# Performance work log

Hardware: AMD Instinct MI355X
Metric: run time of the kernel (lower is better)

The kernel has to match this reference:

```python
import jax, jax.numpy as jnp
import numpy as np

B, S, D_IN, D_OUT = 4, 2048, 1024, 1024

def setup_inputs() -> dict:
    key = jax.random.key(0)
    ks = jax.random.split(key, 6)
    s = 1.0 / np.sqrt(D_IN)
    return {
        "inputs": jax.random.normal(ks[0], (B, S, D_IN), dtype=jnp.float32),
        "Wq": jax.random.normal(ks[1], (D_IN, D_OUT), dtype=jnp.float32) * s,
        "Wk": jax.random.normal(ks[2], (D_IN, D_OUT), dtype=jnp.float32) * s,
        "Wv": jax.random.normal(ks[3], (D_IN, D_OUT), dtype=jnp.float32) * s,
        "Wo": jax.random.normal(ks[4], (D_OUT, D_OUT), dtype=jnp.float32) * (1.0 / np.sqrt(D_OUT)),
        "bo": jax.random.normal(ks[5], (D_OUT,), dtype=jnp.float32) * 0.01,
    }

def reference(inputs, Wq, Wk, Wv, Wo, bo):
    # QKV projections (no bias, matching qkv_bias=False)
    q = inputs @ Wq  # [B,S,D]
    k = inputs @ Wk
    v = inputs @ Wv
    # naive full attention: scores [B,S,S]
    scores = jnp.einsum('bqd,bkd->bqk', q, k) / jnp.sqrt(jnp.asarray(k.shape[-1], q.dtype))
    attn = jax.nn.softmax(scores, axis=-1)
    out = jnp.einsum('bqk,bkd->bqd', attn, v)
    return out @ Wo + bo
```

## Files before the change

kernel.cpp:

```cpp
#include <hip/hip_runtime.h>
#include <hip/hip_bf16.h>
#include <cstdint>

typedef __attribute__((ext_vector_type(8))) __bf16 bf16x8;
typedef __attribute__((ext_vector_type(4))) float  f32x4;

__device__ __forceinline__ unsigned short f2bf(float x) {
    union { float f; unsigned u; } v; v.f = x;
    unsigned r = v.u + 0x7fffu + ((v.u >> 16) & 1u);
    return (unsigned short)(r >> 16);
}
__device__ __forceinline__ unsigned pack2bf(float a, float b) {
    return (unsigned)f2bf(a) | ((unsigned)f2bf(b) << 16);
}

__device__ __forceinline__ void gld_lds16(const unsigned short* g, unsigned short* l) {
    __builtin_amdgcn_global_load_lds(
        (const __attribute__((address_space(1))) unsigned int*)g,
        (__attribute__((address_space(3))) unsigned int*)l,
        16, 0, 0);
}

__global__ void cvt_kernel(const float* __restrict__ in, unsigned short* __restrict__ out, int n4) {
    int i = blockIdx.x * blockDim.x + threadIdx.x;
    if (i < n4) {
        float4 f = ((const float4*)in)[i];
        ushort4 o;
        o.x = f2bf(f.x); o.y = f2bf(f.y); o.z = f2bf(f.z); o.w = f2bf(f.w);
        ((ushort4*)out)[i] = o;
    }
}

__global__ void wpack_kernel(const float* __restrict__ W, unsigned short* __restrict__ out) {
    int tid  = threadIdx.x;
    int lane = tid & 63;
    int chunk = blockIdx.x * 4 + (tid >> 6);
    int nt = chunk >> 5, k32 = chunk & 31;
    int r = lane & 15, q = lane >> 4;
    const float* src = W + (size_t)(k32*32 + q*8) * 1024 + nt*16 + r;
    unsigned o[4];
#pragma unroll
    for (int i = 0; i < 4; i++)
        o[i] = pack2bf(src[(size_t)(2*i) * 1024], src[(size_t)(2*i+1) * 1024]);
    *(uint4*)(out + (size_t)chunk * 512 + lane * 8) = make_uint4(o[0], o[1], o[2], o[3]);
}

__global__ void softmax_kernel(unsigned short* __restrict__ S) {
    const size_t row = blockIdx.x;
    unsigned short* p = S + row * 2048;
    const int tid = threadIdx.x;
    const int wave = tid >> 6, lane = tid & 63;

    uint4 raw = ((const uint4*)p)[tid];
    unsigned u[4] = {raw.x, raw.y, raw.z, raw.w};
    float x[8];
#pragma unroll
    for (int i = 0; i < 4; i++) {
        x[2*i]   = __uint_as_float(u[i] << 16);
        x[2*i+1] = __uint_as_float(u[i] & 0xffff0000u);
    }
    float m = x[0];
#pragma unroll
    for (int i = 1; i < 8; i++) m = fmaxf(m, x[i]);
#pragma unroll
    for (int off = 32; off >= 1; off >>= 1) m = fmaxf(m, __shfl_xor(m, off, 64));
    __shared__ float sm[4], ss[4];
    if (lane == 0) sm[wave] = m;
    __syncthreads();
    m = fmaxf(fmaxf(sm[0], sm[1]), fmaxf(sm[2], sm[3]));

    float e[8], s = 0.f;
#pragma unroll
    for (int i = 0; i < 8; i++) { e[i] = __expf(x[i] - m); s += e[i]; }
#pragma unroll
    for (int off = 32; off >= 1; off >>= 1) s += __shfl_xor(s, off, 64);
    if (lane == 0) ss[wave] = s;
    __syncthreads();
    s = ss[0] + ss[1] + ss[2] + ss[3];
    float inv = 1.0f / s;

    unsigned o[4];
#pragma unroll
    for (int i = 0; i < 4; i++)
        o[i] = pack2bf(e[2*i] * inv, e[2*i+1] * inv);
    ((uint4*)p)[tid] = make_uint4(o[0], o[1], o[2], o[3]);
}

template<int EPI>
__global__ __launch_bounds__(512, 2)
void gemm_pk(const unsigned short* __restrict__ A, const unsigned short* __restrict__ Bpk,
             void* __restrict__ C, unsigned short* __restrict__ Ck, unsigned short* __restrict__ Cv,
             const float* __restrict__ bias,
             int lda, int ldc, int KS, int ns, float scale,
             long long sA, long long sB, long long sC)
{
    __shared__ __align__(16) char smem[98304];

    const int tid  = threadIdx.x;
    const int lane = tid & 63;
    const int wave = tid >> 6;
    const int bz = blockIdx.z;
    A   += (size_t)bz * sA;
    Bpk += (size_t)bz * sB;

    const int gx = gridDim.x;
    int lin = blockIdx.y * gx + blockIdx.x;
    int cpx = (gx * gridDim.y) >> 3;
    int swz = (lin & 7) * cpx + (lin >> 3);
    const int bm = (swz / gx) * 256;
    const int bn = (swz % gx) * 128;

    const int srow = tid >> 2;
    const int scol = ((tid & 3) ^ ((tid >> 3) & 3)) * 8;
    const unsigned short* pa0 = A + (size_t)(bm + srow) * lda + scol;
    const unsigned short* pa1 = pa0 + 32;
    const unsigned short* pa2 = A + (size_t)(bm + 128 + srow) * lda + scol;
    const unsigned short* pa3 = pa2 + 32;

    const int wm = (wave & 3) * 64;
    const int wn = (wave >> 2) * 64;
    const int ln15 = lane & 15;
    const int quad = lane >> 4;
    const int fko = (quad ^ ((ln15 >> 1) & 3)) * 8;
    const int rbase = (wm >> 7) * 4096 + (wm & 127) * 32;
    const int ldsoff = tid * 16;

    const unsigned short* pb[4];
#pragma unroll
    for (int j = 0; j < 4; j++)
        pb[j] = Bpk + (size_t)(((bn + wn + j*16) >> 4) * KS) * 512 + lane * 8;

    f32x4 acc[4][4];
#pragma unroll
    for (int i = 0; i < 4; i++)
#pragma unroll
        for (int j = 0; j < 4; j++) acc[i][j] = (f32x4){0.f, 0.f, 0.f, 0.f};

    auto dma = [&](int buf) {
        char* base = smem + buf * 32768;
        gld_lds16(pa0, (unsigned short*)(base + ldsoff));
        gld_lds16(pa2, (unsigned short*)(base + 8192  + ldsoff));
        gld_lds16(pa1, (unsigned short*)(base + 16384 + ldsoff));
        gld_lds16(pa3, (unsigned short*)(base + 24576 + ldsoff));
        pa0 += 64; pa1 += 64; pa2 += 64; pa3 += 64;
    };
    auto loadB = [&](bf16x8* br) {
#pragma unroll
        for (int j = 0; j < 4; j++) {
            br[j]     = *(const bf16x8*)(pb[j]);
            br[4 + j] = *(const bf16x8*)(pb[j] + 512);
            pb[j] += 1024;
        }
    };
    auto phase = [&](const unsigned short* As, int t, const bf16x8* br) {
        bf16x8 af[4];
#pragma unroll
        for (int i = 0; i < 4; i++)
            af[i] = *(const bf16x8*)&As[t*8192 + rbase + i*512 + ln15*32 + fko];
        __builtin_amdgcn_s_setprio(1);
#pragma unroll
        for (int i = 0; i < 4; i++)
#pragma unroll
            for (int j = 0; j < 4; j++)
                acc[i][j] = __builtin_amdgcn_mfma_f32_16x16x32_bf16(
                    af[i], br[t*4 + j], acc[i][j], 0, 0, 0);
        __builtin_amdgcn_s_setprio(0);
    };

#define SB __builtin_amdgcn_sched_barrier(0)
    bf16x8 b0[8], b1[8];
    SB; dma(0); SB; loadB(b0); SB; dma(1); SB;

    int p = 0;
    for (int it = 0; it < ns; it += 2) {
        const unsigned short* As0 = (const unsigned short*)(smem + p * 32768);
        int p1 = p + 1; if (p1 >= 3) p1 -= 3;
        int q0 = p + 2; if (q0 >= 3) q0 -= 3;
        const unsigned short* As1 = (const unsigned short*)(smem + p1 * 32768);
        const bool more = (it + 2 < ns);

        asm volatile("s_waitcnt vmcnt(12)" ::: "memory");
        SB; __builtin_amdgcn_s_barrier(); SB;
        loadB(b1); SB;
        phase(As0, 0, b0);
        __builtin_amdgcn_s_barrier(); SB;
        if (more) { dma(q0); SB; }
        phase(As0, 1, b0);

        if (more) { asm volatile("s_waitcnt vmcnt(12)" ::: "memory"); }
        else      { asm volatile("s_waitcnt vmcnt(8)"  ::: "memory"); }
        SB; __builtin_amdgcn_s_barrier(); SB;
        if (more) { loadB(b0); SB; }
        phase(As1, 0, b1);
        __builtin_amdgcn_s_barrier(); SB;
        if (it + 3 < ns) { dma(p); SB; }
        phase(As1, 1, b1);

        p = q0;
    }
#undef SB

    if (EPI == 0) {
        float bval[4];
#pragma unroll
        for (int j = 0; j < 4; j++) bval[j] = bias[bn + wn + j*16 + ln15];
        float* Co = (float*)C + (size_t)bz * sC;
#pragma unroll
        for (int i = 0; i < 4; i++) {
            int r0 = bm + wm + i*16 + quad*4;
#pragma unroll
            for (int j = 0; j < 4; j++) {
                int c = bn + wn + j*16 + ln15;
#pragma unroll
                for (int r = 0; r < 4; r++)
                    Co[(size_t)(r0 + r) * ldc + c] = acc[i][j][r] * scale + bval[j];
            }
        }
    } else if (EPI == 1) {
        __syncthreads();
        float* ep = (float*)(smem + wave * 4352);
        unsigned short* Co = (unsigned short*)C + (size_t)bz * sC;
#pragma unroll
        for (int i = 0; i < 4; i++) {
#pragma unroll
            for (int j = 0; j < 4; j++)
#pragma unroll
                for (int r = 0; r < 4; r++)
                    ep[(quad*4 + r) * 68 + j*16 + ln15] = acc[i][j][r] * scale;
            __builtin_amdgcn_s_waitcnt(0);
#pragma unroll
            for (int pp = 0; pp < 2; pp++) {
                int lrow = pp*8 + (lane >> 3);
                int col0 = (lane & 7) * 8;
                float4 lo = *(const float4*)&ep[lrow * 68 + col0];
                float4 hi = *(const float4*)&ep[lrow * 68 + col0 + 4];
                uint4 o;
                o.x = pack2bf(lo.x, lo.y); o.y = pack2bf(lo.z, lo.w);
                o.z = pack2bf(hi.x, hi.y); o.w = pack2bf(hi.z, hi.w);
                *(uint4*)&Co[(size_t)(bm + wm + i*16 + lrow) * ldc + bn + wn + col0] = o;
            }
            __builtin_amdgcn_s_waitcnt(0);
        }
    } else {
        __syncthreads();
        float* ep = (float*)(smem + wave * 8704);
        const int region = bn >> 10;
#pragma unroll
        for (int half = 0; half < 2; half++) {
#pragma unroll
            for (int ii = 0; ii < 2; ii++) {
                int i = half*2 + ii;
#pragma unroll
                for (int j = 0; j < 4; j++)
#pragma unroll
                    for (int r = 0; r < 4; r++)
                        ep[(ii*16 + quad*4 + r) * 68 + j*16 + ln15] = acc[i][j][r] * scale;
            }
            __builtin_amdgcn_s_waitcnt(0);
            const int mrow0 = bm + wm + half*32;
            if (region == 0) {
                unsigned short* Q = (unsigned short*)C;
#pragma unroll
                for (int pp = 0; pp < 4; pp++) {
                    int lrow = pp*8 + (lane >> 3);
                    int col0 = (lane & 7) * 8;
                    float4 lo = *(const float4*)&ep[lrow * 68 + col0];
                    float4 hi = *(const float4*)&ep[lrow * 68 + col0 + 4];
                    uint4 o;
                    o.x = pack2bf(lo.x, lo.y); o.y = pack2bf(lo.z, lo.w);
                    o.z = pack2bf(hi.x, hi.y); o.w = pack2bf(hi.z, hi.w);
                    *(uint4*)&Q[(size_t)(mrow0 + lrow) * ldc + bn + wn + col0] = o;
                }
            } else if (region == 1) {
#pragma unroll
                for (int mt = 0; mt < 2; mt++)
#pragma unroll
                    for (int c = 0; c < 2; c++) {
                        float4 f0 = *(const float4*)&ep[(mt*16 + ln15) * 68 + c*32 + quad*8];
                        float4 f1 = *(const float4*)&ep[(mt*16 + ln15) * 68 + c*32 + quad*8 + 4];
                        uint4 o;
                        o.x = pack2bf(f0.x, f0.y); o.y = pack2bf(f0.z, f0.w);
                        o.z = pack2bf(f1.x, f1.y); o.w = pack2bf(f1.z, f1.w);
                        int cid = ((mrow0 + mt*16) >> 4) * 32 + ((bn - 1024 + wn + c*32) >> 5);
                        *(uint4*)(Ck + (size_t)cid * 512 + lane * 8) = o;
                    }
            } else {
                int s32 = mrow0 >> 5;
#pragma unroll
                for (int dt = 0; dt < 4; dt++) {
                    float v[8];
#pragma unroll
                    for (int e = 0; e < 8; e++)
                        v[e] = ep[(quad*8 + e) * 68 + dt*16 + ln15];
                    uint4 o;
                    o.x = pack2bf(v[0], v[1]); o.y = pack2bf(v[2], v[3]);
                    o.z = pack2bf(v[4], v[5]); o.w = pack2bf(v[6], v[7]);
                    int cid = (((bn - 2048 + wn) >> 4) + dt) * 256 + s32;
                    *(uint4*)(Cv + (size_t)cid * 512 + lane * 8) = o;
                }
            }
            __builtin_amdgcn_s_waitcnt(0);
        }
    }
}

extern "C" void kernel_launch(void* const* d_in, const int* in_sizes, int n_in,
                              void* d_out, int out_size, void* d_ws, size_t ws_size,
                              hipStream_t stream) {
    const float* X  = (const float*)d_in[0];
    const float* Wq = (const float*)d_in[1];
    const float* Wk = (const float*)d_in[2];
    const float* Wv = (const float*)d_in[3];
    const float* Wo = (const float*)d_in[4];
    const float* bo = (const float*)d_in[5];
    float* out = (float*)d_out;

    size_t off = 0;
    auto alloc = [&](size_t bytes) {
        void* p = (char*)d_ws + off;
        off += (bytes + 255) & ~(size_t)255;
        return p;
    };
    unsigned short* Xbf  = (unsigned short*)alloc(8192ull * 1024 * 2);
    unsigned short* Wpk  = (unsigned short*)alloc(192ull * 32 * 512 * 2);
    unsigned short* Wopk = (unsigned short*)alloc(64ull * 32 * 512 * 2);
    unsigned short* Qrm  = (unsigned short*)alloc(8192ull * 1024 * 2);
    unsigned short* Kpk  = (unsigned short*)alloc(512ull * 32 * 512 * 2);
    unsigned short* Vpk  = (unsigned short*)alloc(64ull * 256 * 512 * 2);
    unsigned short* Sc   = (unsigned short*)alloc(4ull * 2048 * 2048 * 2);
    unsigned short* AO   = Xbf;

    cvt_kernel<<<(8192*1024/4 + 255)/256, 256, 0, stream>>>(X, Xbf, 8192*1024/4);
    wpack_kernel<<<512, 256, 0, stream>>>(Wq, Wpk);
    wpack_kernel<<<512, 256, 0, stream>>>(Wk, Wpk + 64*32*512);
    wpack_kernel<<<512, 256, 0, stream>>>(Wv, Wpk + 128*32*512);
    wpack_kernel<<<512, 256, 0, stream>>>(Wo, Wopk);

    gemm_pk<2><<<dim3(3072/128, 8192/256, 1), 512, 0, stream>>>(
        Xbf, Wpk, Qrm, Kpk, Vpk, nullptr, 1024, 1024, 32, 16, 1.0f, 0, 0, 0);

    gemm_pk<1><<<dim3(2048/128, 2048/256, 4), 512, 0, stream>>>(
        Qrm, Kpk, Sc, nullptr, nullptr, nullptr, 1024, 2048, 32, 16, 0.03125f,
        2048ll*1024, 128ll*32*512, 2048ll*2048);

    softmax_kernel<<<8192, 256, 0, stream>>>(Sc);

    gemm_pk<1><<<dim3(1024/128, 2048/256, 4), 512, 0, stream>>>(
        Sc, Vpk, AO, nullptr, nullptr, nullptr, 2048, 1024, 256, 32, 1.0f,
        2048ll*2048, 64ll*512, 2048ll*1024);

    gemm_pk<0><<<dim3(1024/128, 8192/256, 1), 512, 0, stream>>>(
        AO, Wopk, out, nullptr, nullptr, bo, 1024, 1024, 32, 16, 1.0f, 0, 0, 0);

    (void)n_in; (void)in_sizes; (void)out_size; (void)ws_size;
}
```

Measured before the change: 301.9 us.

## Use 256x256 tiles with LDS-staged B for QKV and score GEMMs

Adds a new GEMM kernel, gemm8p, with 256x256 block tiles. Each wave computes a 128x64 sub-tile, and both A and B are staged into a double-buffered 128KB LDS through direct global-to-LDS loads, where before B was loaded into registers from global memory. The QKV projection and QK^T score GEMMs now use this kernel; the PV and output GEMMs keep the old one. The larger tile raises arithmetic intensity and cuts redundant A/B traffic, but doubles the accumulator registers and raises LDS use to 128KB, which may limit occupancy to one block per CU and shrinks the grid.

After: 284.4 us. -5.8%, faster.

```diff
diff --git a/kernel.cpp b/kernel.cpp
--- a/kernel.cpp
+++ b/kernel.cpp
@@ -88,13 +88,12 @@
 
 template<int EPI>
 __global__ __launch_bounds__(512, 2)
-void gemm_pk(const unsigned short* __restrict__ A, const unsigned short* __restrict__ Bpk,
-             void* __restrict__ C, unsigned short* __restrict__ Ck, unsigned short* __restrict__ Cv,
-             const float* __restrict__ bias,
-             int lda, int ldc, int KS, int ns, float scale,
-             long long sA, long long sB, long long sC)
+void gemm8p(const unsigned short* __restrict__ A, const unsigned short* __restrict__ Bpk,
+            void* __restrict__ C, unsigned short* __restrict__ Ck, unsigned short* __restrict__ Cv,
+            int lda, int ldc, int KS, int ns, float scale,
+            long long sA, long long sB, long long sC)
 {
-    __shared__ __align__(16) char smem[98304];
+    __shared__ __align__(16) char smem[131072];
 
     const int tid  = threadIdx.x;
     const int lane = tid & 63;
@@ -108,120 +107,90 @@
     int cpx = (gx * gridDim.y) >> 3;
     int swz = (lin & 7) * cpx + (lin >> 3);
     const int bm = (swz / gx) * 256;
-    const int bn = (swz % gx) * 128;
-
-    const int srow = tid >> 2;
-    const int scol = ((tid & 3) ^ ((tid >> 3) & 3)) * 8;
-    const unsigned short* pa0 = A + (size_t)(bm + srow) * lda + scol;
-    const unsigned short* pa1 = pa0 + 32;
-    const unsigned short* pa2 = A + (size_t)(bm + 128 + srow) * lda + scol;
-    const unsigned short* pa3 = pa2 + 32;
-
-    const int wm = (wave & 3) * 64;
-    const int wn = (wave >> 2) * 64;
+    const int bn = (swz % gx) * 256;
+
+    const int wm = (wave & 1) * 128;
+    const int wn = (wave >> 1) * 64;
     const int ln15 = lane & 15;
     const int quad = lane >> 4;
     const int fko = (quad ^ ((ln15 >> 1) & 3)) * 8;
-    const int rbase = (wm >> 7) * 4096 + (wm & 127) * 32;
-    const int ldsoff = tid * 16;
-
-    const unsigned short* pb[4];
-#pragma unroll
-    for (int j = 0; j < 4; j++)
-        pb[j] = Bpk + (size_t)(((bn + wn + j*16) >> 4) * KS) * 512 + lane * 8;
-
-    f32x4 acc[4][4];
-#pragma unroll
-    for (int i = 0; i < 4; i++)
+
+    const int srow = tid >> 2;
+    const int scol = ((tid & 3) ^ ((tid >> 3) & 3)) * 8;
+    const unsigned short* paU = A + (size_t)(bm + srow) * lda + scol;
+    const unsigned short* paL = A + (size_t)(bm + 128 + srow) * lda + scol;
+    const unsigned short* pb0 = Bpk + (size_t)((bn >> 4) + (tid >> 6)) * KS * 512 + lane * 8;
+    const long long pbstep = (long long)8 * KS * 512;
+
+    f32x4 acc[8][4];
+#pragma unroll
+    for (int i = 0; i < 8; i++)
 #pragma unroll
         for (int j = 0; j < 4; j++) acc[i][j] = (f32x4){0.f, 0.f, 0.f, 0.f};
 
-    auto dma = [&](int buf) {
-        char* base = smem + buf * 32768;
-        gld_lds16(pa0, (unsigned short*)(base + ldsoff));
-        gld_lds16(pa2, (unsigned short*)(base + 8192  + ldsoff));
-        gld_lds16(pa1, (unsigned short*)(base + 16384 + ldsoff));
-        gld_lds16(pa3, (unsigned short*)(base + 24576 + ldsoff));
-        pa0 += 64; pa1 += 64; pa2 += 64; pa3 += 64;
-    };
-    auto loadB = [&](bf16x8* br) {
-#pragma unroll
-        for (int j = 0; j < 4; j++) {
-            br[j]     = *(const bf16x8*)(pb[j]);
-            br[4 + j] = *(const bf16x8*)(pb[j] + 512);
-            pb[j] += 1024;
-        }
-    };
-    auto phase = [&](const unsigned short* As, int t, const bf16x8* br) {
-        bf16x8 af[4];
+    auto stageA = [&](int buf, int t, int k) {
+        char* d = smem + buf * 32768 + k * 16384 + tid * 16;
+        const unsigned short* s = paU + t * 64 + k * 32;
+        gld_lds16(s, (unsigned short*)d);
+        gld_lds16(paL + t * 64 + k * 32, (unsigned short*)(d + 8192));
+    };
+    auto stageB = [&](int buf, int t, int k) {
+        char* d = smem + 65536 + buf * 32768 + k * 16384 + (tid >> 6) * 1024 + lane * 16;
+        const unsigned short* s = pb0 + (size_t)(2 * t + k) * 512;
+        gld_lds16(s, (unsigned short*)d);
+        gld_lds16(s + pbstep, (unsigned short*)(d + 8192));
+    };
+    auto phase = [&](int buf, int k, int mh) {
+        const unsigned short* Ar = (const unsigned short*)(smem + buf * 32768 + k * 16384);
+        const unsigned short* Br = (const unsigned short*)(smem + 65536 + buf * 32768 + k * 16384);
+        bf16x8 af[4], bf[4];
 #pragma unroll
         for (int i = 0; i < 4; i++)
-            af[i] = *(const bf16x8*)&As[t*8192 + rbase + i*512 + ln15*32 + fko];
+            af[i] = *(const bf16x8*)&Ar[(wm + mh * 64 + i * 16 + ln15) * 32 + fko];
+#pragma unroll
+        for (int j = 0; j < 4; j++)
+            bf[j] = *(const bf16x8*)&Br[((wn >> 4) + j) * 512 + lane * 8];
         __builtin_amdgcn_s_setprio(1);
 #pragma unroll
         for (int i = 0; i < 4; i++)
 #pragma unroll
             for (int j = 0; j < 4; j++)
-                acc[i][j] = __builtin_amdgcn_mfma_f32_16x16x32_bf16(
-                    af[i], br[t*4 + j], acc[i][j], 0, 0, 0);
+                acc[mh * 4 + i][j] = __builtin_amdgcn_mfma_f32_16x16x32_bf16(
+                    af[i], bf[j], acc[mh * 4 + i][j], 0, 0, 0);
         __builtin_amdgcn_s_setprio(0);
     };
 
-#define SB __builtin_amdgcn_sched_barrier(0)
-    bf16x8 b0[8], b1[8];
-    SB; dma(0); SB; loadB(b0); SB; dma(1); SB;
-
-    int p = 0;
-    for (int it = 0; it < ns; it += 2) {
-        const unsigned short* As0 = (const unsigned short*)(smem + p * 32768);
-        int p1 = p + 1; if (p1 >= 3) p1 -= 3;
-        int q0 = p + 2; if (q0 >= 3) q0 -= 3;
-        const unsigned short* As1 = (const unsigned short*)(smem + p1 * 32768);
-        const bool more = (it + 2 < ns);
-
-        asm volatile("s_waitcnt vmcnt(12)" ::: "memory");
-        SB; __builtin_amdgcn_s_barrier(); SB;
-        loadB(b1); SB;
-        phase(As0, 0, b0);
-        __builtin_amdgcn_s_barrier(); SB;
-        if (more) { dma(q0); SB; }
-        phase(As0, 1, b0);
-
-        if (more) { asm volatile("s_waitcnt vmcnt(12)" ::: "memory"); }
-        else      { asm volatile("s_waitcnt vmcnt(8)"  ::: "memory"); }
-        SB; __builtin_amdgcn_s_barrier(); SB;
-        if (more) { loadB(b0); SB; }
-        phase(As1, 0, b1);
-        __builtin_amdgcn_s_barrier(); SB;
-        if (it + 3 < ns) { dma(p); SB; }
-        phase(As1, 1, b1);
-
-        p = q0;
+#define SB  __builtin_amdgcn_sched_barrier(0)
+#define FEN asm volatile("" ::: "memory")
+    stageB(0, 0, 0); stageA(0, 0, 0); stageB(0, 0, 1); stageA(0, 0, 1); SB;
+
+    for (int t = 0; t < ns; ++t) {
+        const int buf = t & 1, nb = buf ^ 1;
+        const int tn = (t + 1 < ns) ? t + 1 : 0;
+        asm volatile("s_waitcnt vmcnt(4)" ::: "memory");
+        __builtin_amdgcn_s_barrier(); FEN;
+        stageB(nb, tn, 0); SB;
+        phase(buf, 0, 0);
+        __builtin_amdgcn_s_barrier(); FEN;
+        stageA(nb, tn, 0); SB;
+        phase(buf, 0, 1);
+        asm volatile("s_waitcnt vmcnt(4)" ::: "memory");
+        __builtin_amdgcn_s_barrier(); FEN;
+        stageB(nb, tn, 1); SB;
+        phase(buf, 1, 0);
+        __builtin_amdgcn_s_barrier(); FEN;
+        stageA(nb, tn, 1); SB;
+        phase(buf, 1, 1);
     }
 #undef SB
-
-    if (EPI == 0) {
-        float bval[4];
-#pragma unroll
-        for (int j = 0; j < 4; j++) bval[j] = bias[bn + wn + j*16 + ln15];
-        float* Co = (float*)C + (size_t)bz * sC;
-#pragma unroll
-        for (int i = 0; i < 4; i++) {
-            int r0 = bm + wm + i*16 + quad*4;
-#pragma unroll
-            for (int j = 0; j < 4; j++) {
-                int c = bn + wn + j*16 + ln15;
-#pragma unroll
-                for (int r = 0; r < 4; r++)
-                    Co[(size_t)(r0 + r) * ldc + c] = acc[i][j][r] * scale + bval[j];
-            }
-        }
-    } else if (EPI == 1) {
+#undef FEN
+
+    if (EPI == 1) {
         __syncthreads();
         float* ep = (float*)(smem + wave * 4352);
         unsigned short* Co = (unsigned short*)C + (size_t)bz * sC;
 #pragma unroll
-        for (int i = 0; i < 4; i++) {
+        for (int i = 0; i < 8; i++) {
 #pragma unroll
             for (int j = 0; j < 4; j++)
 #pragma unroll
@@ -246,10 +215,10 @@
         float* ep = (float*)(smem + wave * 8704);
         const int region = bn >> 10;
 #pragma unroll
-        for (int half = 0; half < 2; half++) {
+        for (int g = 0; g < 4; g++) {
 #pragma unroll
             for (int ii = 0; ii < 2; ii++) {
-                int i = half*2 + ii;
+                int i = g*2 + ii;
 #pragma unroll
                 for (int j = 0; j < 4; j++)
 #pragma unroll
@@ -257,7 +226,7 @@
                         ep[(ii*16 + quad*4 + r) * 68 + j*16 + ln15] = acc[i][j][r] * scale;
             }
             __builtin_amdgcn_s_waitcnt(0);
-            const int mrow0 = bm + wm + half*32;
+            const int mrow0 = bm + wm + g*32;
             if (region == 0) {
                 unsigned short* Q = (unsigned short*)C;
 #pragma unroll
@@ -304,6 +273,164 @@
     }
 }
 
+template<int EPI>
+__global__ __launch_bounds__(512, 2)
+void gemm_pk(const unsigned short* __restrict__ A, const unsigned short* __restrict__ Bpk,
+             void* __restrict__ C, unsigned short* __restrict__ Ck, unsigned short* __restrict__ Cv,
+             const float* __restrict__ bias,
+             int lda, int ldc, int KS, int ns, float scale,
+             long long sA, long long sB, long long sC)
+{
+    __shared__ __align__(16) char smem[98304];
+
+    const int tid  = threadIdx.x;
+    const int lane = tid & 63;
+    const int wave = tid >> 6;
+    const int bz = blockIdx.z;
+    A   += (size_t)bz * sA;
+    Bpk += (size_t)bz * sB;
+
+    const int gx = gridDim.x;
+    int lin = blockIdx.y * gx + blockIdx.x;
+    int cpx = (gx * gridDim.y) >> 3;
+    int swz = (lin & 7) * cpx + (lin >> 3);
+    const int bm = (swz / gx) * 256;
+    const int bn = (swz % gx) * 128;
+
+    const int srow = tid >> 2;
+    const int scol = ((tid & 3) ^ ((tid >> 3) & 3)) * 8;
+    const unsigned short* pa0 = A + (size_t)(bm + srow) * lda + scol;
+    const unsigned short* pa1 = pa0 + 32;
+    const unsigned short* pa2 = A + (size_t)(bm + 128 + srow) * lda + scol;
+    const unsigned short* pa3 = pa2 + 32;
+
+    const int wm = (wave & 3) * 64;
+    const int wn = (wave >> 2) * 64;
+    const int ln15 = lane & 15;
+    const int quad = lane >> 4;
+    const int fko = (quad ^ ((ln15 >> 1) & 3)) * 8;
+    const int rbase = (wm >> 7) * 4096 + (wm & 127) * 32;
+    const int ldsoff = tid * 16;
+
+    const unsigned short* pb[4];
+#pragma unroll
+    for (int j = 0; j < 4; j++)
+        pb[j] = Bpk + (size_t)(((bn + wn + j*16) >> 4) * KS) * 512 + lane * 8;
+
+    f32x4 acc[4][4];
+#pragma unroll
+    for (int i = 0; i < 4; i++)
+#pragma unroll
+        for (int j = 0; j < 4; j++) acc[i][j] = (f32x4){0.f, 0.f, 0.f, 0.f};
+
+    auto dma = [&](int buf) {
+        char* base = smem + buf * 32768;
+        gld_lds16(pa0, (unsigned short*)(base + ldsoff));
+        gld_lds16(pa2, (unsigned short*)(base + 8192  + ldsoff));
+        gld_lds16(pa1, (unsigned short*)(base + 16384 + ldsoff));
+        gld_lds16(pa3, (unsigned short*)(base + 24576 + ldsoff));
+        pa0 += 64; pa1 += 64; pa2 += 64; pa3 += 64;
+    };
+    auto loadB = [&](bf16x8* br) {
+#pragma unroll
+        for (int j = 0; j < 4; j++) {
+            br[j]     = *(const bf16x8*)(pb[j]);
+            br[4 + j] = *(const bf16x8*)(pb[j] + 512);
+            pb[j] += 1024;
+        }
+    };
+    auto phase = [&](const unsigned short* As, int t, const bf16x8* br) {
+        bf16x8 af[4];
+#pragma unroll
+        for (int i = 0; i < 4; i++)
+            af[i] = *(const bf16x8*)&As[t*8192 + rbase + i*512 + ln15*32 + fko];
+        __builtin_amdgcn_s_setprio(1);
+#pragma unroll
+        for (int i = 0; i < 4; i++)
+#pragma unroll
+            for (int j = 0; j < 4; j++)
+                acc[i][j] = __builtin_amdgcn_mfma_f32_16x16x32_bf16(
+                    af[i], br[t*4 + j], acc[i][j], 0, 0, 0);
+        __builtin_amdgcn_s_setprio(0);
+    };
+
+#define SB __builtin_amdgcn_sched_barrier(0)
+    bf16x8 b0[8], b1[8];
+    SB; dma(0); SB; loadB(b0); SB; dma(1); SB;
+
+    int p = 0;
+    for (int it = 0; it < ns; it += 2) {
+        const unsigned short* As0 = (const unsigned short*)(smem + p * 32768);
+        int p1 = p + 1; if (p1 >= 3) p1 -= 3;
+        int q0 = p + 2; if (q0 >= 3) q0 -= 3;
+        const unsigned short* As1 = (const unsigned short*)(smem + p1 * 32768);
+        const bool more = (it + 2 < ns);
+
+        asm volatile("s_waitcnt vmcnt(12)" ::: "memory");
+        SB; __builtin_amdgcn_s_barrier(); SB;
+        loadB(b1); SB;
+        phase(As0, 0, b0);
+        __builtin_amdgcn_s_barrier(); SB;
+        if (more) { dma(q0); SB; }
+        phase(As0, 1, b0);
+
+        if (more) { asm volatile("s_waitcnt vmcnt(12)" ::: "memory"); }
+        else      { asm volatile("s_waitcnt vmcnt(8)"  ::: "memory"); }
+        SB; __builtin_amdgcn_s_barrier(); SB;
+        if (more) { loadB(b0); SB; }
+        phase(As1, 0, b1);
+        __builtin_amdgcn_s_barrier(); SB;
+        if (it + 3 < ns) { dma(p); SB; }
+        phase(As1, 1, b1);
+
+        p = q0;
+    }
+#undef SB
+
+    if (EPI == 0) {
+        float bval[4];
+#pragma unroll
+        for (int j = 0; j < 4; j++) bval[j] = bias[bn + wn + j*16 + ln15];
+        float* Co = (float*)C + (size_t)bz * sC;
+#pragma unroll
+        for (int i = 0; i < 4; i++) {
+            int r0 = bm + wm + i*16 + quad*4;
+#pragma unroll
+            for (int j = 0; j < 4; j++) {
+                int c = bn + wn + j*16 + ln15;
+#pragma unroll
+                for (int r = 0; r < 4; r++)
+                    Co[(size_t)(r0 + r) * ldc + c] = acc[i][j][r] * scale + bval[j];
+            }
+        }
+    } else if (EPI == 1) {
+        __syncthreads();
+        float* ep = (float*)(smem + wave * 4352);
+        unsigned short* Co = (unsigned short*)C + (size_t)bz * sC;
+#pragma unroll
+        for (int i = 0; i < 4; i++) {
+#pragma unroll
+            for (int j = 0; j < 4; j++)
+#pragma unroll
+                for (int r = 0; r < 4; r++)
+                    ep[(quad*4 + r) * 68 + j*16 + ln15] = acc[i][j][r] * scale;
+            __builtin_amdgcn_s_waitcnt(0);
+#pragma unroll
+            for (int pp = 0; pp < 2; pp++) {
+                int lrow = pp*8 + (lane >> 3);
+                int col0 = (lane & 7) * 8;
+                float4 lo = *(const float4*)&ep[lrow * 68 + col0];
+                float4 hi = *(const float4*)&ep[lrow * 68 + col0 + 4];
+                uint4 o;
+                o.x = pack2bf(lo.x, lo.y); o.y = pack2bf(lo.z, lo.w);
+                o.z = pack2bf(hi.x, hi.y); o.w = pack2bf(hi.z, hi.w);
+                *(uint4*)&Co[(size_t)(bm + wm + i*16 + lrow) * ldc + bn + wn + col0] = o;
+            }
+            __builtin_amdgcn_s_waitcnt(0);
+        }
+    }
+}
+
 extern "C" void kernel_launch(void* const* d_in, const int* in_sizes, int n_in,
                               void* d_out, int out_size, void* d_ws, size_t ws_size,
                               hipStream_t stream) {
@@ -336,11 +463,11 @@
     wpack_kernel<<<512, 256, 0, stream>>>(Wv, Wpk + 128*32*512);
     wpack_kernel<<<512, 256, 0, stream>>>(Wo, Wopk);
 
-    gemm_pk<2><<<dim3(3072/128, 8192/256, 1), 512, 0, stream>>>(
-        Xbf, Wpk, Qrm, Kpk, Vpk, nullptr, 1024, 1024, 32, 16, 1.0f, 0, 0, 0);
-
-    gemm_pk<1><<<dim3(2048/128, 2048/256, 4), 512, 0, stream>>>(
-        Qrm, Kpk, Sc, nullptr, nullptr, nullptr, 1024, 2048, 32, 16, 0.03125f,
+    gemm8p<2><<<dim3(3072/256, 8192/256, 1), 512, 0, stream>>>(
+        Xbf, Wpk, Qrm, Kpk, Vpk, 1024, 1024, 32, 16, 1.0f, 0, 0, 0);
+
+    gemm8p<1><<<dim3(2048/256, 2048/256, 4), 512, 0, stream>>>(
+        Qrm, Kpk, Sc, nullptr, nullptr, 1024, 2048, 32, 16, 0.03125f,
         2048ll*1024, 128ll*32*512, 2048ll*2048);
 
     softmax_kernel<<<8192, 256, 0, stream>>>(Sc);
```
